# Kernel optimization log

Hardware: AMD Instinct MI355X
Metric: run time of the kernel (lower is better)

Reference implementation:

```python
import jax, jax.numpy as jnp
import numpy as np

N = 8192        # n_nodes == in_features (forced by elementwise input * W)
F_OUT = 128     # out_features
ALPHA = 0.2     # LeakyReLU negative slope
NEG_BIG = -9.0e15


def setup_inputs() -> dict:
    key = jax.random.key(0)
    k1, k2, k3, k4, k5 = jax.random.split(key, 5)
    x = jax.random.normal(k1, (N, F_OUT), dtype=jnp.float32)
    adj = jax.random.randint(k2, (N, N), 0, 2, dtype=jnp.int32)
    # xavier_uniform-style params
    W = jax.random.uniform(k3, (N, F_OUT), dtype=jnp.float32, minval=-1.0, maxval=1.0) * np.float32(1.414 * np.sqrt(6.0 / (N + F_OUT)))
    a = jax.random.uniform(k4, (2 * F_OUT, 1), dtype=jnp.float32, minval=-1.0, maxval=1.0) * np.float32(1.414 * np.sqrt(6.0 / (2 * F_OUT + 1)))
    W2 = jax.random.uniform(k5, (N, 1), dtype=jnp.float32, minval=-1.0, maxval=1.0) * np.float32(1.414 * np.sqrt(6.0 / (N + 1)))
    return {"x": x, "adj": adj, "W": W, "a": a, "W2": W2}


def reference(x, adj, W, a, W2):
    # h = input * W  (elementwise, shapes [N, F])
    h = x * W
    f = W.shape[1]
    # e[i,j] = leakyrelu( concat(h[i], h[j]) @ a ) = leakyrelu(h[i]@a1 + h[j]@a2)
    f1 = h @ a[:f]        # [N, 1]
    f2 = h @ a[f:]        # [N, 1]
    e = jax.nn.leaky_relu(f1 + f2.T, negative_slope=ALPHA)  # [N, N]
    e = jnp.where(adj > 0, e, NEG_BIG)
    attention = jax.nn.softmax(e, axis=1)  # dropout rate = 0.0 -> no-op
    h_prime = attention @ h                # [N, F] (stored as side effect in original)
    # output path: elu( (adj @ W2).T @ x ).T  -> [F, 1]
    adj_f = adj.astype(x.dtype)
    h_prime_3 = ((adj_f @ W2).T @ x).T     # [F, 1]
    out = jax.nn.elu(h_prime_3)            # concat=True branch
    return out, h_prime
```

## Files before the change

### kernel.cpp

```cpp
#include <hip/hip_runtime.h>
#include <hip/hip_bf16.h>

#define ALPHA 0.2f

typedef __attribute__((ext_vector_type(8)))  __bf16 bf16x8;
typedef int          i32x4 __attribute__((ext_vector_type(4)));
typedef float        f32x4 __attribute__((ext_vector_type(4)));
typedef unsigned int u32x4 __attribute__((ext_vector_type(4)));

static __device__ __forceinline__ unsigned short bf16bits(float v) {
    __bf16 b = (__bf16)v;
    unsigned short u;
    __builtin_memcpy(&u, &b, 2);
    return u;
}

__global__ __launch_bounds__(256) void gat_prep(
    const float* __restrict__ x, const float* __restrict__ W, const float* __restrict__ a,
    float* __restrict__ f1, float* __restrict__ f2, unsigned short* __restrict__ hB,
    float* __restrict__ ws_acc)
{
    __shared__ unsigned short lh[32][136];
    int t = threadIdx.x;
    int i0 = blockIdx.x * 32;
    if (blockIdx.x == 0 && t < 128) ws_acc[t] = 0.0f;

    int row = t >> 3, q = t & 7;
    int i = i0 + row;
    const float4* xp  = (const float4*)(x + (size_t)i * 128 + q * 16);
    const float4* wp  = (const float4*)(W + (size_t)i * 128 + q * 16);
    const float4* a1p = (const float4*)(a + q * 16);
    const float4* a2p = (const float4*)(a + 128 + q * 16);
    float p1 = 0.f, p2 = 0.f;
    #pragma unroll
    for (int jj = 0; jj < 4; ++jj) {
        float4 xv = xp[jj], wv = wp[jj], a1v = a1p[jj], a2v = a2p[jj];
        float h0 = xv.x * wv.x, h1 = xv.y * wv.y, h2 = xv.z * wv.z, h3 = xv.w * wv.w;
        p1 += h0 * a1v.x + h1 * a1v.y + h2 * a1v.z + h3 * a1v.w;
        p2 += h0 * a2v.x + h1 * a2v.y + h2 * a2v.z + h3 * a2v.w;
        int fb = q * 16 + jj * 4;
        lh[row][fb + 0] = bf16bits(h0);
        lh[row][fb + 1] = bf16bits(h1);
        lh[row][fb + 2] = bf16bits(h2);
        lh[row][fb + 3] = bf16bits(h3);
    }
    p1 += __shfl_xor(p1, 1); p1 += __shfl_xor(p1, 2); p1 += __shfl_xor(p1, 4);
    p2 += __shfl_xor(p2, 1); p2 += __shfl_xor(p2, 2); p2 += __shfl_xor(p2, 4);
    if (q == 0) { f1[i] = p1; f2[i] = p2; }
    __syncthreads();

    int ftl = t >> 5, s0 = t & 31;
    size_t fragbase = ((size_t)blockIdx.x * 8 + ftl) * 512;
    #pragma unroll
    for (int hw = 0; hw < 2; ++hw) {
        int s = s0 + hw * 32;
        int jl = (s >> 4) * 8;
        int f = ftl * 16 + (s & 15);
        unsigned int p[4];
        #pragma unroll
        for (int k = 0; k < 4; ++k) {
            unsigned int lo = lh[jl + 2 * k][f];
            unsigned int hi = lh[jl + 2 * k + 1][f];
            p[k] = lo | (hi << 16);
        }
        u32x4 v = {p[0], p[1], p[2], p[3]};
        *(u32x4*)(hB + fragbase + s * 8) = v;
    }
}

__global__ __launch_bounds__(256, 2) void gat_main(
    const int* __restrict__ adj, const float* __restrict__ x,
    const float* __restrict__ W2, const float* __restrict__ f1g,
    const float* __restrict__ f2g, const unsigned short* __restrict__ hB,
    float* __restrict__ hp_part, float* __restrict__ den_part,
    float* __restrict__ ws_acc)
{
    __shared__ unsigned short tile[4][16][264];
    __shared__ float den_s[4][16], rs_s[4][16];

    int tid = threadIdx.x;
    int w = tid >> 6, l = tid & 63;
    int gid = blockIdx.x >> 1, jh = blockIdx.x & 1;
    int i0 = gid * 16;

    float f1r[16];
    #pragma unroll
    for (int r = 0; r < 16; ++r) f1r[r] = f1g[i0 + r];

    float den[16], rs[16];
    #pragma unroll
    for (int r = 0; r < 16; ++r) { den[r] = 0.f; rs[r] = 0.f; }
    f32x4 acc[8] = {};

    const int jbase0 = jh * 4096 + w * 1024;
    const int* arow = adj + (size_t)i0 * 8192 + jbase0 + l * 4;
    const float* f2p = f2g + jbase0 + l * 4;
    const float* w2p = W2 + jbase0 + l * 4;

    i32x4 adjreg[16];
    f32x4 f2v, w2v;
    auto issue = [&](int c) {
        int jo = c * 256;
        f2v = *(const f32x4*)(f2p + jo);
        w2v = *(const f32x4*)(w2p + jo);
        #pragma unroll
        for (int r = 0; r < 16; ++r)
            adjreg[r] = __builtin_nontemporal_load(
                (const i32x4*)(arow + (size_t)r * 8192 + jo));
    };
    issue(0);

    const unsigned short* hBw = hB + (size_t)jbase0 * 128 + l * 8;
    const unsigned short* ap  = &tile[w][l & 15][(l >> 4) * 8];

    for (int c = 0; c < 4; ++c) {
        #pragma unroll
        for (int r = 0; r < 16; ++r) {
            i32x4 ad = adjreg[r];
            float g[4];
            float dsum = 0.f, rsum = 0.f;
            #pragma unroll
            for (int e = 0; e < 4; ++e) {
                float tt = f1r[r] + f2v[e];
                float lr = fmaxf(tt, ALPHA * tt);
                float ex = __expf(lr);
                float gg = (ad[e] != 0) ? ex : 0.0f;
                g[e] = gg;
                dsum += gg;
                rsum += (ad[e] != 0) ? w2v[e] : 0.0f;
            }
            den[r] += dsum;
            rs[r] += rsum;
            unsigned int p0 = bf16bits(g[0]) | ((unsigned int)bf16bits(g[1]) << 16);
            unsigned int p1 = bf16bits(g[2]) | ((unsigned int)bf16bits(g[3]) << 16);
            *(uint2*)&tile[w][r][l * 4] = make_uint2(p0, p1);
        }
        if (c < 3) issue(c + 1);

        const unsigned short* bp = hBw + (size_t)c * 32768;
        bf16x8 bbuf[2][8];
        #pragma unroll
        for (int ft = 0; ft < 8; ++ft)
            bbuf[0][ft] = *(const bf16x8*)(bp + ft * 512);
        #pragma unroll
        for (int ksl = 0; ksl < 8; ++ksl) {
            int cur = ksl & 1;
            if (ksl < 7) {
                const unsigned short* bk = bp + (size_t)(ksl + 1) * 4096;
                #pragma unroll
                for (int ft = 0; ft < 8; ++ft)
                    bbuf[cur ^ 1][ft] = *(const bf16x8*)(bk + ft * 512);
            }
            bf16x8 af = *(const bf16x8*)(ap + ksl * 32);
            #pragma unroll
            for (int ft = 0; ft < 8; ++ft)
                acc[ft] = __builtin_amdgcn_mfma_f32_16x16x32_bf16(af, bbuf[cur][ft], acc[ft], 0, 0, 0);
        }
    }

    #pragma unroll
    for (int r = 0; r < 16; ++r) {
        float d = den[r], rr = rs[r];
        #pragma unroll
        for (int off = 1; off < 64; off <<= 1) {
            d += __shfl_xor(d, off);
            rr += __shfl_xor(rr, off);
        }
        if (l == 0) { den_s[w][r] = d; rs_s[w][r] = rr; }
    }

    __syncthreads();

    float* av = (float*)acc;
    if (w != 0) {
        float* dst = (float*)&tile[0][0][0] + (size_t)(w - 1) * 2048;
        #pragma unroll
        for (int j = 0; j < 32; ++j) dst[j * 64 + l] = av[j];
    }
    __syncthreads();

    if (w == 0) {
        #pragma unroll
        for (int ww = 0; ww < 3; ++ww) {
            const float* srcp = (const float*)&tile[0][0][0] + (size_t)ww * 2048;
            #pragma unroll
            for (int j = 0; j < 32; ++j) av[j] += srcp[j * 64 + l];
        }
        int q = l >> 4, col = l & 15;
        float* hpb = hp_part + ((size_t)jh * 8192 + i0) * 128;
        #pragma unroll
        for (int ft = 0; ft < 8; ++ft) {
            #pragma unroll
            for (int reg = 0; reg < 4; ++reg) {
                int row = q * 4 + reg;
                __builtin_nontemporal_store(acc[ft][reg],
                    hpb + (size_t)row * 128 + ft * 16 + col);
            }
        }
        if (l < 16) {
            float dsum = den_s[0][l] + den_s[1][l] + den_s[2][l] + den_s[3][l];
            den_part[(size_t)jh * 8192 + i0 + l] = dsum;
        }
    } else if (w == 1) {
        float px = 0.f, py = 0.f;
        #pragma unroll
        for (int r = 0; r < 16; ++r) {
            float rm = rs_s[0][r] + rs_s[1][r] + rs_s[2][r] + rs_s[3][r];
            const float* xr = x + (size_t)(i0 + r) * 128;
            px += rm * xr[l];
            py += rm * xr[l + 64];
        }
        atomicAdd(ws_acc + l, px);
        atomicAdd(ws_acc + l + 64, py);
    }
}

__global__ __launch_bounds__(256) void gat_norm(
    const float* __restrict__ hp_part, const float* __restrict__ den_part,
    float* __restrict__ hp)
{
    int t = threadIdx.x;
    int row = blockIdx.x * 32 + (t >> 3);
    int f0 = (t & 7) * 16;
    float d = den_part[row] + den_part[8192 + row];
    float inv = (d != 0.f) ? 1.0f / d : 0.f;
    const f32x4* p0 = (const f32x4*)(hp_part + (size_t)row * 128 + f0);
    const f32x4* p1 = (const f32x4*)(hp_part + (size_t)(8192 + row) * 128 + f0);
    f32x4* o = (f32x4*)(hp + (size_t)row * 128 + f0);
    #pragma unroll
    for (int k = 0; k < 4; ++k) {
        f32x4 v = (p0[k] + p1[k]);
        o[k] = v * inv;
    }
}

__global__ __launch_bounds__(128) void gat_finish(const float* __restrict__ ws_acc,
                                                  float* __restrict__ out)
{
    int t = threadIdx.x;
    float v = ws_acc[t];
    out[t] = (v > 0.f) ? v : (__expf(v) - 1.0f);
}

extern "C" void kernel_launch(void* const* d_in, const int* in_sizes, int n_in,
                              void* d_out, int out_size, void* d_ws, size_t ws_size,
                              hipStream_t stream) {
    const float* x   = (const float*)d_in[0];
    const int*   adj = (const int*)d_in[1];
    const float* W   = (const float*)d_in[2];
    const float* a   = (const float*)d_in[3];
    const float* W2  = (const float*)d_in[4];
    float* out = (float*)d_out;

    float* wsf     = (float*)d_ws;
    float* ws_acc  = wsf;
    float* f1      = wsf + 128;
    float* f2      = wsf + 128 + 8192;
    unsigned short* hB = (unsigned short*)(wsf + 128 + 2 * 8192);
    float* hp_part = wsf + 128 + 2 * 8192 + 524288;
    float* den_part = hp_part + 2 * 8192 * 128;

    gat_prep<<<256, 256, 0, stream>>>(x, W, a, f1, f2, hB, ws_acc);
    gat_main<<<1024, 256, 0, stream>>>(adj, x, W2, f1, f2, hB, hp_part, den_part, ws_acc);
    gat_norm<<<256, 256, 0, stream>>>(hp_part, den_part, out + 128);
    gat_finish<<<1, 128, 0, stream>>>(ws_acc, out);
}
```

Before: 395.8 us.

## Process 32 rows per block, halving hB reloads, and compute softmax denominator via MFMA

Each gat_main block now handles 32 query rows instead of 16, so every loaded hB fragment feeds two MFMA row tiles, and the grid shrinks to 512 blocks. Each adjacency load is narrowed to two ints per lane across eight chunks. The denominator is computed by an extra MFMA against a ones vector, using the same bf16-rounded weights as the numerator, which removes the per-row shuffle reductions. f1 values are made wave-uniform with readfirstlane. The cost is higher register pressure (32 f1 values, 32 adjacency pairs, two accumulator sets), fewer blocks, a serialized three-step cross-wave reduction with extra barriers, and narrower loads.

```diff
diff --git a/kernel.cpp b/kernel.cpp
--- a/kernel.cpp
+++ b/kernel.cpp
@@ -4,7 +4,8 @@
 #define ALPHA 0.2f
 
 typedef __attribute__((ext_vector_type(8)))  __bf16 bf16x8;
-typedef int          i32x4 __attribute__((ext_vector_type(4)));
+typedef int          i32x2 __attribute__((ext_vector_type(2)));
+typedef float        f32x2 __attribute__((ext_vector_type(2)));
 typedef float        f32x4 __attribute__((ext_vector_type(4)));
 typedef unsigned int u32x4 __attribute__((ext_vector_type(4)));
 
@@ -75,136 +76,153 @@
     float* __restrict__ hp_part, float* __restrict__ den_part,
     float* __restrict__ ws_acc)
 {
-    __shared__ unsigned short tile[4][16][264];
-    __shared__ float den_s[4][16], rs_s[4][16];
+    __shared__ unsigned short tile[4][32][136];
+    __shared__ float rs_s[4][32];
 
     int tid = threadIdx.x;
     int w = tid >> 6, l = tid & 63;
     int gid = blockIdx.x >> 1, jh = blockIdx.x & 1;
-    int i0 = gid * 16;
-
-    float f1r[16];
-    #pragma unroll
-    for (int r = 0; r < 16; ++r) f1r[r] = f1g[i0 + r];
-
-    float den[16], rs[16];
-    #pragma unroll
-    for (int r = 0; r < 16; ++r) { den[r] = 0.f; rs[r] = 0.f; }
-    f32x4 acc[8] = {};
-
-    const int jbase0 = jh * 4096 + w * 1024;
-    const int* arow = adj + (size_t)i0 * 8192 + jbase0 + l * 4;
-    const float* f2p = f2g + jbase0 + l * 4;
-    const float* w2p = W2 + jbase0 + l * 4;
-
-    i32x4 adjreg[16];
-    f32x4 f2v, w2v;
+    int i0 = gid * 32;
+
+    float f1r[32];
+    #pragma unroll
+    for (int r = 0; r < 32; ++r)
+        f1r[r] = __uint_as_float(__builtin_amdgcn_readfirstlane(__float_as_uint(f1g[i0 + r])));
+
+    float rs[32];
+    #pragma unroll
+    for (int r = 0; r < 32; ++r) rs[r] = 0.f;
+    f32x4 acc[2][8] = {};
+    f32x4 accd[2] = {};
+
+    const int jbase = jh * 4096 + w * 1024;
+    const int* arow = adj + (size_t)i0 * 8192 + jbase + l * 2;
+    const float* f2p = f2g + jbase + l * 2;
+    const float* w2p = W2 + jbase + l * 2;
+
+    i32x2 adjreg[32];
+    f32x2 f2v, w2v;
     auto issue = [&](int c) {
-        int jo = c * 256;
-        f2v = *(const f32x4*)(f2p + jo);
-        w2v = *(const f32x4*)(w2p + jo);
-        #pragma unroll
-        for (int r = 0; r < 16; ++r)
+        int jo = c * 128;
+        f2v = *(const f32x2*)(f2p + jo);
+        w2v = *(const f32x2*)(w2p + jo);
+        #pragma unroll
+        for (int r = 0; r < 32; ++r)
             adjreg[r] = __builtin_nontemporal_load(
-                (const i32x4*)(arow + (size_t)r * 8192 + jo));
+                (const i32x2*)(arow + (size_t)r * 8192 + jo));
     };
     issue(0);
 
-    const unsigned short* hBw = hB + (size_t)jbase0 * 128 + l * 8;
-    const unsigned short* ap  = &tile[w][l & 15][(l >> 4) * 8];
-
-    for (int c = 0; c < 4; ++c) {
-        #pragma unroll
-        for (int r = 0; r < 16; ++r) {
-            i32x4 ad = adjreg[r];
-            float g[4];
-            float dsum = 0.f, rsum = 0.f;
-            #pragma unroll
-            for (int e = 0; e < 4; ++e) {
-                float tt = f1r[r] + f2v[e];
+    bf16x8 ones;
+    #pragma unroll
+    for (int e = 0; e < 8; ++e) ones[e] = (__bf16)1.0f;
+
+    const unsigned short* hBw = hB + (size_t)jbase * 128 + l * 8;
+    const unsigned short* ap0 = &tile[w][l & 15][(l >> 4) * 8];
+    const unsigned short* ap1 = &tile[w][16 + (l & 15)][(l >> 4) * 8];
+
+    for (int c = 0; c < 8; ++c) {
+        f32x2 cf2 = f2v, cw2 = w2v;
+        #pragma unroll
+        for (int r = 0; r < 32; ++r) {
+            i32x2 ad = adjreg[r];
+            float g[2];
+            #pragma unroll
+            for (int e = 0; e < 2; ++e) {
+                float tt = f1r[r] + cf2[e];
                 float lr = fmaxf(tt, ALPHA * tt);
                 float ex = __expf(lr);
                 float gg = (ad[e] != 0) ? ex : 0.0f;
                 g[e] = gg;
-                dsum += gg;
-                rsum += (ad[e] != 0) ? w2v[e] : 0.0f;
-            }
-            den[r] += dsum;
-            rs[r] += rsum;
-            unsigned int p0 = bf16bits(g[0]) | ((unsigned int)bf16bits(g[1]) << 16);
-            unsigned int p1 = bf16bits(g[2]) | ((unsigned int)bf16bits(g[3]) << 16);
-            *(uint2*)&tile[w][r][l * 4] = make_uint2(p0, p1);
-        }
-        if (c < 3) issue(c + 1);
-
-        const unsigned short* bp = hBw + (size_t)c * 32768;
-        bf16x8 bbuf[2][8];
-        #pragma unroll
-        for (int ft = 0; ft < 8; ++ft)
-            bbuf[0][ft] = *(const bf16x8*)(bp + ft * 512);
-        #pragma unroll
-        for (int ksl = 0; ksl < 8; ++ksl) {
-            int cur = ksl & 1;
-            if (ksl < 7) {
-                const unsigned short* bk = bp + (size_t)(ksl + 1) * 4096;
+                rs[r] += (ad[e] != 0) ? cw2[e] : 0.0f;
+            }
+            unsigned int pk = bf16bits(g[0]) | ((unsigned int)bf16bits(g[1]) << 16);
+            *(unsigned int*)&tile[w][r][l * 2] = pk;
+        }
+        if (c < 7) issue(c + 1);
+
+        const unsigned short* bp = hBw + (size_t)c * 16384;
+        bf16x8 bbuf[2][4];
+        #pragma unroll
+        for (int q = 0; q < 4; ++q)
+            bbuf[0][q] = *(const bf16x8*)(bp + q * 512);
+        bf16x8 af0, af1;
+        #pragma unroll
+        for (int hi = 0; hi < 8; ++hi) {
+            int cur = hi & 1;
+            if (hi < 7) {
+                const unsigned short* nb = bp + (size_t)((hi + 1) >> 1) * 4096
+                                              + (size_t)((hi + 1) & 1) * 2048;
+                #pragma unroll
+                for (int q = 0; q < 4; ++q)
+                    bbuf[cur ^ 1][q] = *(const bf16x8*)(nb + q * 512);
+            }
+            if ((hi & 1) == 0) {
+                int ks = hi >> 1;
+                af0 = *(const bf16x8*)(ap0 + ks * 32);
+                af1 = *(const bf16x8*)(ap1 + ks * 32);
+                accd[0] = __builtin_amdgcn_mfma_f32_16x16x32_bf16(af0, ones, accd[0], 0, 0, 0);
+                accd[1] = __builtin_amdgcn_mfma_f32_16x16x32_bf16(af1, ones, accd[1], 0, 0, 0);
+            }
+            #pragma unroll
+            for (int q = 0; q < 4; ++q) {
+                int ftg = (hi & 1) * 4 + q;
+                acc[0][ftg] = __builtin_amdgcn_mfma_f32_16x16x32_bf16(af0, bbuf[cur][q], acc[0][ftg], 0, 0, 0);
+                acc[1][ftg] = __builtin_amdgcn_mfma_f32_16x16x32_bf16(af1, bbuf[cur][q], acc[1][ftg], 0, 0, 0);
+            }
+        }
+    }
+
+    #pragma unroll
+    for (int r = 0; r < 32; ++r) {
+        float rr = rs[r];
+        #pragma unroll
+        for (int off = 1; off < 64; off <<= 1) rr += __shfl_xor(rr, off);
+        if (l == 0) rs_s[w][r] = rr;
+    }
+
+    __syncthreads();
+    float* fb = (float*)&tile[0][0][0];
+    float* av = (float*)acc;
+    float* avd = (float*)accd;
+    #pragma unroll 1
+    for (int wsrc = 1; wsrc < 4; ++wsrc) {
+        if (w == wsrc) {
+            #pragma unroll
+            for (int j = 0; j < 64; ++j) fb[j * 64 + l] = av[j];
+            #pragma unroll
+            for (int j = 0; j < 8; ++j) fb[(64 + j) * 64 + l] = avd[j];
+        }
+        __syncthreads();
+        if (w == 0) {
+            #pragma unroll
+            for (int j = 0; j < 64; ++j) av[j] += fb[j * 64 + l];
+            #pragma unroll
+            for (int j = 0; j < 8; ++j) avd[j] += fb[(64 + j) * 64 + l];
+        }
+        __syncthreads();
+    }
+
+    if (w == 0) {
+        int q = l >> 4, col = l & 15;
+        float* hpb = hp_part + ((size_t)jh * 8192 + i0) * 128;
+        #pragma unroll
+        for (int m = 0; m < 2; ++m) {
+            #pragma unroll
+            for (int reg = 0; reg < 4; ++reg) {
+                int row = m * 16 + q * 4 + reg;
                 #pragma unroll
                 for (int ft = 0; ft < 8; ++ft)
-                    bbuf[cur ^ 1][ft] = *(const bf16x8*)(bk + ft * 512);
-            }
-            bf16x8 af = *(const bf16x8*)(ap + ksl * 32);
-            #pragma unroll
-            for (int ft = 0; ft < 8; ++ft)
-                acc[ft] = __builtin_amdgcn_mfma_f32_16x16x32_bf16(af, bbuf[cur][ft], acc[ft], 0, 0, 0);
-        }
-    }
-
-    #pragma unroll
-    for (int r = 0; r < 16; ++r) {
-        float d = den[r], rr = rs[r];
-        #pragma unroll
-        for (int off = 1; off < 64; off <<= 1) {
-            d += __shfl_xor(d, off);
-            rr += __shfl_xor(rr, off);
-        }
-        if (l == 0) { den_s[w][r] = d; rs_s[w][r] = rr; }
-    }
-
-    __syncthreads();
-
-    float* av = (float*)acc;
-    if (w != 0) {
-        float* dst = (float*)&tile[0][0][0] + (size_t)(w - 1) * 2048;
-        #pragma unroll
-        for (int j = 0; j < 32; ++j) dst[j * 64 + l] = av[j];
-    }
-    __syncthreads();
-
-    if (w == 0) {
-        #pragma unroll
-        for (int ww = 0; ww < 3; ++ww) {
-            const float* srcp = (const float*)&tile[0][0][0] + (size_t)ww * 2048;
-            #pragma unroll
-            for (int j = 0; j < 32; ++j) av[j] += srcp[j * 64 + l];
-        }
-        int q = l >> 4, col = l & 15;
-        float* hpb = hp_part + ((size_t)jh * 8192 + i0) * 128;
-        #pragma unroll
-        for (int ft = 0; ft < 8; ++ft) {
-            #pragma unroll
-            for (int reg = 0; reg < 4; ++reg) {
-                int row = q * 4 + reg;
-                __builtin_nontemporal_store(acc[ft][reg],
-                    hpb + (size_t)row * 128 + ft * 16 + col);
-            }
-        }
-        if (l < 16) {
-            float dsum = den_s[0][l] + den_s[1][l] + den_s[2][l] + den_s[3][l];
-            den_part[(size_t)jh * 8192 + i0 + l] = dsum;
+                    __builtin_nontemporal_store(acc[m][ft][reg],
+                        hpb + (size_t)row * 128 + ft * 16 + col);
+                if (col == 0)
+                    den_part[(size_t)jh * 8192 + i0 + row] = accd[m][reg];
+            }
         }
     } else if (w == 1) {
         float px = 0.f, py = 0.f;
         #pragma unroll
-        for (int r = 0; r < 16; ++r) {
+        for (int r = 0; r < 32; ++r) {
             float rm = rs_s[0][r] + rs_s[1][r] + rs_s[2][r] + rs_s[3][r];
             const float* xr = x + (size_t)(i0 + r) * 128;
             px += rm * xr[l];
@@ -261,7 +279,7 @@
     float* den_part = hp_part + 2 * 8192 * 128;
 
     gat_prep<<<256, 256, 0, stream>>>(x, W, a, f1, f2, hB, ws_acc);
-    gat_main<<<1024, 256, 0, stream>>>(adj, x, W2, f1, f2, hB, hp_part, den_part, ws_acc);
+    gat_main<<<512, 256, 0, stream>>>(adj, x, W2, f1, f2, hB, hp_part, den_part, ws_acc);
     gat_norm<<<256, 256, 0, stream>>>(hp_part, den_part, out + 128);
     gat_finish<<<1, 128, 0, stream>>>(ws_acc, out);
 }
```

After: 428.5 us. 8.3% more time.

## Use 512-thread blocks covering 64 rows with each wave spanning 2048 columns

Applied to the files above, without the earlier changes.

The main kernel goes from 1024 blocks of 256 threads, each handling 16 rows, to 256 blocks of 512 threads, each handling 64 rows. Each wave now owns 16 rows and 2048 columns over eight chunks, so only pairs of waves reduce through LDS, and there are a quarter as many x-weighted atomics and less reduction overhead. The grid now matches the CU count in a single wave of blocks. In exchange, the launch bound of 512 threads with min 2 blocks per CU cuts the register budget per thread, which risks spilling the large adj and B-fragment register buffers. The serial 64-row loop in one wave also gets longer.

```diff
diff --git a/kernel.cpp b/kernel.cpp
--- a/kernel.cpp
+++ b/kernel.cpp
@@ -68,34 +68,36 @@
     }
 }
 
-__global__ __launch_bounds__(256, 2) void gat_main(
+__global__ __launch_bounds__(512, 2) void gat_main(
     const int* __restrict__ adj, const float* __restrict__ x,
     const float* __restrict__ W2, const float* __restrict__ f1g,
     const float* __restrict__ f2g, const unsigned short* __restrict__ hB,
     float* __restrict__ hp_part, float* __restrict__ den_part,
     float* __restrict__ ws_acc)
 {
-    __shared__ unsigned short tile[4][16][264];
-    __shared__ float den_s[4][16], rs_s[4][16];
+    __shared__ unsigned short tile[8][16][264];
+    __shared__ float den_s[8][16], rs_s[8][16];
 
     int tid = threadIdx.x;
     int w = tid >> 6, l = tid & 63;
+    int mg = w >> 1, js = w & 1;
     int gid = blockIdx.x >> 1, jh = blockIdx.x & 1;
-    int i0 = gid * 16;
+    int i0 = gid * 64;
+    int iw = i0 + mg * 16;
 
     float f1r[16];
     #pragma unroll
-    for (int r = 0; r < 16; ++r) f1r[r] = f1g[i0 + r];
+    for (int r = 0; r < 16; ++r) f1r[r] = f1g[iw + r];
 
     float den[16], rs[16];
     #pragma unroll
     for (int r = 0; r < 16; ++r) { den[r] = 0.f; rs[r] = 0.f; }
     f32x4 acc[8] = {};
 
-    const int jbase0 = jh * 4096 + w * 1024;
-    const int* arow = adj + (size_t)i0 * 8192 + jbase0 + l * 4;
-    const float* f2p = f2g + jbase0 + l * 4;
-    const float* w2p = W2 + jbase0 + l * 4;
+    const int jbase = jh * 4096 + js * 2048;
+    const int* arow = adj + (size_t)iw * 8192 + jbase + l * 4;
+    const float* f2p = f2g + jbase + l * 4;
+    const float* w2p = W2 + jbase + l * 4;
 
     i32x4 adjreg[16];
     f32x4 f2v, w2v;
@@ -110,10 +112,10 @@
     };
     issue(0);
 
-    const unsigned short* hBw = hB + (size_t)jbase0 * 128 + l * 8;
+    const unsigned short* hBw = hB + (size_t)jbase * 128 + l * 8;
     const unsigned short* ap  = &tile[w][l & 15][(l >> 4) * 8];
 
-    for (int c = 0; c < 4; ++c) {
+    for (int c = 0; c < 8; ++c) {
         #pragma unroll
         for (int r = 0; r < 16; ++r) {
             i32x4 ad = adjreg[r];
@@ -135,7 +137,7 @@
             unsigned int p1 = bf16bits(g[2]) | ((unsigned int)bf16bits(g[3]) << 16);
             *(uint2*)&tile[w][r][l * 4] = make_uint2(p0, p1);
         }
-        if (c < 3) issue(c + 1);
+        if (c < 7) issue(c + 1);
 
         const unsigned short* bp = hBw + (size_t)c * 32768;
         bf16x8 bbuf[2][8];
@@ -171,23 +173,21 @@
 
     __syncthreads();
 
+    float* fb = (float*)&tile[0][0][0];
     float* av = (float*)acc;
-    if (w != 0) {
-        float* dst = (float*)&tile[0][0][0] + (size_t)(w - 1) * 2048;
+    if (js == 1) {
+        float* dst = fb + (size_t)mg * 2048;
         #pragma unroll
         for (int j = 0; j < 32; ++j) dst[j * 64 + l] = av[j];
     }
     __syncthreads();
 
-    if (w == 0) {
-        #pragma unroll
-        for (int ww = 0; ww < 3; ++ww) {
-            const float* srcp = (const float*)&tile[0][0][0] + (size_t)ww * 2048;
-            #pragma unroll
-            for (int j = 0; j < 32; ++j) av[j] += srcp[j * 64 + l];
-        }
+    if (js == 0) {
+        const float* srcp = fb + (size_t)mg * 2048;
+        #pragma unroll
+        for (int j = 0; j < 32; ++j) av[j] += srcp[j * 64 + l];
         int q = l >> 4, col = l & 15;
-        float* hpb = hp_part + ((size_t)jh * 8192 + i0) * 128;
+        float* hpb = hp_part + ((size_t)jh * 8192 + iw) * 128;
         #pragma unroll
         for (int ft = 0; ft < 8; ++ft) {
             #pragma unroll
@@ -197,15 +197,13 @@
                     hpb + (size_t)row * 128 + ft * 16 + col);
             }
         }
-        if (l < 16) {
-            float dsum = den_s[0][l] + den_s[1][l] + den_s[2][l] + den_s[3][l];
-            den_part[(size_t)jh * 8192 + i0 + l] = dsum;
-        }
+        if (l < 16)
+            den_part[(size_t)jh * 8192 + iw + l] = den_s[w][l] + den_s[w + 1][l];
     } else if (w == 1) {
         float px = 0.f, py = 0.f;
-        #pragma unroll
-        for (int r = 0; r < 16; ++r) {
-            float rm = rs_s[0][r] + rs_s[1][r] + rs_s[2][r] + rs_s[3][r];
+        for (int r = 0; r < 64; ++r) {
+            int mgr = r >> 4;
+            float rm = rs_s[mgr * 2][r & 15] + rs_s[mgr * 2 + 1][r & 15];
             const float* xr = x + (size_t)(i0 + r) * 128;
             px += rm * xr[l];
             py += rm * xr[l + 64];
@@ -261,7 +259,7 @@
     float* den_part = hp_part + 2 * 8192 * 128;
 
     gat_prep<<<256, 256, 0, stream>>>(x, W, a, f1, f2, hB, ws_acc);
-    gat_main<<<1024, 256, 0, stream>>>(adj, x, W2, f1, f2, hB, hp_part, den_part, ws_acc);
+    gat_main<<<256, 512, 0, stream>>>(adj, x, W2, f1, f2, hB, hp_part, den_part, ws_acc);
     gat_norm<<<256, 256, 0, stream>>>(hp_part, den_part, out + 128);
     gat_finish<<<1, 128, 0, stream>>>(ws_acc, out);
 }
```

After: 397.5 us. No clear change (+0.4%).
